# Kernel tuning notes

Hardware: AMD Instinct MI355X
Metric: run time of the kernel (lower is better)

## Reference

```python
import jax, jax.numpy as jnp
import numpy as np

N, E = 20000, 320000
IN, HID, H, C, DFF, L = 256, 64, 4, 64, 128, 4  # per-head dim C = out_channels, concat width = H*C


def _init(k, shape, fan):
    return jax.random.normal(k, shape, jnp.float32) / np.float32(np.sqrt(fan))


def setup_inputs() -> dict:
    key = jax.random.key(0)
    ks = jax.random.split(key, 10)
    x = jax.random.normal(ks[0], (N, IN), jnp.float32)
    edge_index = jax.random.randint(ks[1], (2, E), 0, N)
    We = _init(ks[2], (IN, HID), IN)
    be = jnp.zeros((HID,), jnp.float32)
    Wc = _init(ks[3], (L, HID, H * C), HID)
    att_src = _init(ks[4], (L, H, C), C)
    att_dst = _init(ks[5], (L, H, C), C)
    bc = jnp.zeros((L, H * C), jnp.float32)
    W1 = _init(ks[6], (L, H * C, DFF), H * C)
    b1 = jnp.zeros((L, DFF), jnp.float32)
    W2 = _init(ks[7], (L, DFF, HID), DFF)
    b2 = jnp.zeros((L, HID), jnp.float32)
    ln_g = jnp.ones((L, HID), jnp.float32)
    ln_b = jnp.zeros((L, HID), jnp.float32)
    return dict(x=x, edge_index=edge_index, We=We, be=be, Wc=Wc, att_src=att_src,
                att_dst=att_dst, bc=bc, W1=W1, b1=b1, W2=W2, b2=b2, ln_g=ln_g, ln_b=ln_b)


def _layernorm(x, g, b, eps=1e-5):
    m = x.mean(-1, keepdims=True)
    v = ((x - m) ** 2).mean(-1, keepdims=True)
    return (x - m) / jnp.sqrt(v + eps) * g + b


def reference(x, edge_index, We, be, Wc, att_src, att_dst, bc, W1, b1, W2, b2, ln_g, ln_b):
    # dropout omitted (eval mode)
    n = x.shape[0]
    loops = jnp.arange(n, dtype=edge_index.dtype)
    src = jnp.concatenate([edge_index[0], loops])  # GATConv add_self_loops=True
    dst = jnp.concatenate([edge_index[1], loops])
    h = (x @ We + be) * jnp.sqrt(jnp.float32(HID))  # embed * sqrt(hidden)
    for l in range(L):  # small fixed layer loop
        xh = (h @ Wc[l]).reshape(n, H, C)          # [n,H,C]
        a_s = (xh * att_src[l]).sum(-1)            # [n,H]
        a_d = (xh * att_dst[l]).sum(-1)
        e = a_s[src] + a_d[dst]                    # [E+n,H]
        e = jnp.where(e > 0, e, 0.2 * e)           # leaky_relu(0.2)
        m = jax.ops.segment_max(e, dst, num_segments=n)
        e = jnp.exp(e - m[dst])
        z = jax.ops.segment_sum(e, dst, num_segments=n)
        alpha = e / (z[dst] + 1e-16)               # segment softmax over incoming edges
        msg = xh[src] * alpha[:, :, None]          # [E+n,H,C]
        out = jax.ops.segment_sum(msg, dst, num_segments=n).reshape(n, H * C) + bc[l]
        f = jax.nn.gelu(out @ W1[l] + b1[l], approximate=False) @ W2[l] + b2[l]
        h = h + _layernorm(f, ln_g[l], ln_b[l])    # residual
    return h  # last_hidden_state (head is None)
```

## Files before the change

kernel.cpp:

```cpp
#include <hip/hip_runtime.h>
#include <cmath>

#define NN   20000
#define NE   320000
#define IND  256
#define HIDD 64
#define NH   4
#define CD   64
#define HC   256
#define DFFD 128
#define NL   4


static __device__ __forceinline__ float lrelu(float v) { return v > 0.f ? v : 0.2f * v; }
static __device__ __forceinline__ float wsum(float v) { for (int k = 32; k; k >>= 1) v += __shfl_xor(v, k); return v; }
static __device__ __forceinline__ float wmax(float v) { for (int k = 32; k; k >>= 1) v = fmaxf(v, __shfl_xor(v, k)); return v; }

__global__ void ws_kernel(const float* __restrict__ Wc, const float* __restrict__ att_src,
                          const float* __restrict__ att_dst, float* __restrict__ ws_all) {
    int idx = blockIdx.x * 256 + threadIdx.x;
    int l = idx >> 9, r = (idx >> 6) & 7, k = idx & 63;
    int hh = r & 3;
    const float* att = ((r & 4) ? att_dst : att_src) + (size_t)l * NH * CD + hh * CD;
    const float* wrow = Wc + (size_t)l * HIDD * HC + (size_t)k * HC + hh * CD;
    float s = 0.f;
    for (int c = 0; c < CD; ++c) s += wrow[c] * att[c];
    ws_all[idx] = s;
}

__global__ void w1eff_kernel(const float* __restrict__ Wc, const float* __restrict__ W1,
                             float* __restrict__ W1eff) {
    const int b = blockIdx.x;
    const int l = b >> 8, hk = b & 255, hh = hk >> 6, kl = hk & 63;
    const int f = threadIdx.x;
    const float* wc = Wc + (size_t)l * HIDD * HC + (size_t)kl * HC + hh * 64;
    const float* w1 = W1 + (size_t)l * HC * DFFD + (size_t)(hh * 64) * DFFD + f;
    float s = 0.f;
#pragma unroll 4
    for (int c = 0; c < 64; ++c) s += wc[c] * w1[(size_t)c * DFFD];
    W1eff[(size_t)l * HC * DFFD + (size_t)hk * DFFD + f] = s;
}

__global__ void b1eff_kernel(const float* __restrict__ bc, const float* __restrict__ W1,
                             const float* __restrict__ b1, float* __restrict__ b1eff) {
    const int l = blockIdx.x, f = threadIdx.x;
    const float* w1 = W1 + (size_t)l * HC * DFFD + f;
    const float* bcl = bc + (size_t)l * HC;
    float s = b1[(size_t)l * DFFD + f];
    for (int c = 0; c < HC; ++c) s += bcl[c] * w1[(size_t)c * DFFD];
    b1eff[l * DFFD + f] = s;
}

__global__ __launch_bounds__(256) void embed_kernel(const float* __restrict__ x,
                                                    const float* __restrict__ We,
                                                    const float* __restrict__ be,
                                                    const float* __restrict__ ws_all,
                                                    float* __restrict__ h,
                                                    float* __restrict__ a_s, float* __restrict__ a_d) {
    __shared__ float s_x[16 * IND];
    const int base = blockIdx.x * 16, t = threadIdx.x;
    for (int idx = t; idx < 16 * IND / 4; idx += 256)
        ((float4*)s_x)[idx] = ((const float4*)(x + (size_t)base * IND))[idx];
    __syncthreads();
    const int c = t & 63, g = t >> 6;
    float acc[4] = {0.f, 0.f, 0.f, 0.f};
    const float4* sx4 = (const float4*)s_x;
#pragma unroll 2
    for (int k4 = 0; k4 < IND / 4; ++k4) {
        float w0 = We[(4 * k4 + 0) * HIDD + c];
        float w1 = We[(4 * k4 + 1) * HIDD + c];
        float w2 = We[(4 * k4 + 2) * HIDD + c];
        float w3 = We[(4 * k4 + 3) * HIDD + c];
#pragma unroll
        for (int i = 0; i < 4; ++i) {
            float4 v = sx4[(4 * g + i) * (IND / 4) + k4];
            acc[i] += v.x * w0 + v.y * w1 + v.z * w2 + v.w * w3;
        }
    }
    float bias = be[c];
    float wr[8];
#pragma unroll
    for (int r = 0; r < 8; ++r) wr[r] = ws_all[r * 64 + c];
#pragma unroll
    for (int i = 0; i < 4; ++i) {
        int node = base + 4 * g + i;
        float hv = (acc[i] + bias) * 8.0f;
        h[(size_t)node * HIDD + c] = hv;
        float s0 = wsum(hv * wr[0]), s1 = wsum(hv * wr[1]);
        float s2 = wsum(hv * wr[2]), s3 = wsum(hv * wr[3]);
        float s4 = wsum(hv * wr[4]), s5 = wsum(hv * wr[5]);
        float s6 = wsum(hv * wr[6]), s7 = wsum(hv * wr[7]);
        if (c == 0) {
            ((float4*)a_s)[node] = make_float4(s0, s1, s2, s3);
            ((float4*)a_d)[node] = make_float4(s4, s5, s6, s7);
        }
    }
}

__global__ void init_deg(int* __restrict__ deg, int* __restrict__ cursor) {
    int i = blockIdx.x * blockDim.x + threadIdx.x;
    if (i < NN) { deg[i] = 1; cursor[i] = 0; }
}

__global__ void count_edges(const int* __restrict__ ei, int* __restrict__ deg) {
    int e = blockIdx.x * blockDim.x + threadIdx.x;
    if (e < NE) atomicAdd(&deg[ei[NE + e]], 1);
}

__global__ void scan_kernel(const int* __restrict__ deg, int* __restrict__ rowptr) {
    __shared__ int part[1024];
    const int t = threadIdx.x;
    const int CH = (NN + 1023) / 1024;
    int lo = t * CH, hi = lo + CH; if (hi > NN) hi = NN;
    int s = 0;
    for (int i = lo; i < hi; ++i) s += deg[i];
    part[t] = s;
    __syncthreads();
    for (int off = 1; off < 1024; off <<= 1) {
        int v = 0;
        if (t >= off) v = part[t - off];
        __syncthreads();
        if (t >= off) part[t] += v;
        __syncthreads();
    }
    int base = (t == 0) ? 0 : part[t - 1];
    for (int i = lo; i < hi; ++i) { rowptr[i] = base; base += deg[i]; }
    if (lo <= NN - 1 && NN - 1 < hi) rowptr[NN] = base;
}

__global__ void scatter_edges(const int* __restrict__ ei, const int* __restrict__ rowptr,
                              int* __restrict__ cursor, int* __restrict__ csr_src) {
    int e = blockIdx.x * blockDim.x + threadIdx.x;
    if (e < NE) {
        int s = ei[e], d = ei[NE + e];
        int pos = atomicAdd(&cursor[d], 1);
        csr_src[rowptr[d] + pos] = s;
    } else if (e < NE + NN) {
        int i = e - NE;
        int pos = atomicAdd(&cursor[i], 1);
        csr_src[rowptr[i] + pos] = i;
    }
}

__global__ __launch_bounds__(256) void agg_kernel(
    const float* __restrict__ h, const float* __restrict__ a_s, const float* __restrict__ a_d,
    const int* __restrict__ rowptr, const int* __restrict__ csr_src,
    float* __restrict__ hagg) {
    __shared__ int    s_src[8][64];
    __shared__ float4 s_w[8][64];
    const int t = threadIdx.x, wave = t >> 6, lane = t & 63;
    const float4* as4 = (const float4*)a_s;
#pragma unroll
    for (int nd = 0; nd < 2; ++nd) {
        const int slot = wave * 2 + nd;
        const int i = blockIdx.x * 8 + slot;
        const int lo = rowptr[i], n = rowptr[i + 1] - lo;
        const float4 ad = ((const float4*)a_d)[i];
        float acc0 = 0.f, acc1 = 0.f, acc2 = 0.f, acc3 = 0.f;
        if (n <= 64) {
            float e0 = -1e30f, e1 = -1e30f, e2 = -1e30f, e3 = -1e30f;
            if (lane < n) {
                int s = csr_src[lo + lane];
                s_src[slot][lane] = s;
                float4 a = as4[s];
                e0 = lrelu(a.x + ad.x); e1 = lrelu(a.y + ad.y);
                e2 = lrelu(a.z + ad.z); e3 = lrelu(a.w + ad.w);
            }
            float M0 = wmax(e0), M1 = wmax(e1), M2 = wmax(e2), M3 = wmax(e3);
            float p0 = __expf(e0 - M0), p1 = __expf(e1 - M1);
            float p2 = __expf(e2 - M2), p3 = __expf(e3 - M3);
            float iz0 = 1.f / (wsum(p0) + 1e-16f), iz1 = 1.f / (wsum(p1) + 1e-16f);
            float iz2 = 1.f / (wsum(p2) + 1e-16f), iz3 = 1.f / (wsum(p3) + 1e-16f);
            if (lane < n) s_w[slot][lane] = make_float4(p0 * iz0, p1 * iz1, p2 * iz2, p3 * iz3);
            int j = 0;
            for (; j + 4 <= n; j += 4) {
                int  q0 = s_src[slot][j],     q1 = s_src[slot][j + 1];
                int  q2 = s_src[slot][j + 2], q3 = s_src[slot][j + 3];
                float h0 = h[(size_t)q0 * HIDD + lane], h1 = h[(size_t)q1 * HIDD + lane];
                float h2 = h[(size_t)q2 * HIDD + lane], h3 = h[(size_t)q3 * HIDD + lane];
                float4 w0 = s_w[slot][j],     w1 = s_w[slot][j + 1];
                float4 w2 = s_w[slot][j + 2], w3 = s_w[slot][j + 3];
                acc0 += h0 * w0.x + h1 * w1.x + h2 * w2.x + h3 * w3.x;
                acc1 += h0 * w0.y + h1 * w1.y + h2 * w2.y + h3 * w3.y;
                acc2 += h0 * w0.z + h1 * w1.z + h2 * w2.z + h3 * w3.z;
                acc3 += h0 * w0.w + h1 * w1.w + h2 * w2.w + h3 * w3.w;
            }
            for (; j < n; ++j) {
                float hv = h[(size_t)s_src[slot][j] * HIDD + lane];
                float4 w = s_w[slot][j];
                acc0 += hv * w.x; acc1 += hv * w.y; acc2 += hv * w.z; acc3 += hv * w.w;
            }
        } else {
            float m0 = -1e30f, m1 = -1e30f, m2 = -1e30f, m3 = -1e30f;
            for (int j = lane; j < n; j += 64) {
                int s = csr_src[lo + j];
                float4 a = as4[s];
                m0 = fmaxf(m0, lrelu(a.x + ad.x)); m1 = fmaxf(m1, lrelu(a.y + ad.y));
                m2 = fmaxf(m2, lrelu(a.z + ad.z)); m3 = fmaxf(m3, lrelu(a.w + ad.w));
            }
            m0 = wmax(m0); m1 = wmax(m1); m2 = wmax(m2); m3 = wmax(m3);
            float z0 = 0.f, z1 = 0.f, z2 = 0.f, z3 = 0.f;
            for (int j = lane; j < n; j += 64) {
                int s = csr_src[lo + j];
                float4 a = as4[s];
                z0 += __expf(lrelu(a.x + ad.x) - m0); z1 += __expf(lrelu(a.y + ad.y) - m1);
                z2 += __expf(lrelu(a.z + ad.z) - m2); z3 += __expf(lrelu(a.w + ad.w) - m3);
            }
            float iz0 = 1.f / (wsum(z0) + 1e-16f), iz1 = 1.f / (wsum(z1) + 1e-16f);
            float iz2 = 1.f / (wsum(z2) + 1e-16f), iz3 = 1.f / (wsum(z3) + 1e-16f);
            for (int cb = 0; cb < n; cb += 64) {
                int nn = n - cb; if (nn > 64) nn = 64;
                if (lane < nn) {
                    int s = csr_src[lo + cb + lane];
                    s_src[slot][lane] = s;
                    float4 a = as4[s];
                    s_w[slot][lane] = make_float4(__expf(lrelu(a.x + ad.x) - m0) * iz0,
                                                  __expf(lrelu(a.y + ad.y) - m1) * iz1,
                                                  __expf(lrelu(a.z + ad.z) - m2) * iz2,
                                                  __expf(lrelu(a.w + ad.w) - m3) * iz3);
                }
                int j = 0;
                for (; j + 4 <= nn; j += 4) {
                    int  q0 = s_src[slot][j],     q1 = s_src[slot][j + 1];
                    int  q2 = s_src[slot][j + 2], q3 = s_src[slot][j + 3];
                    float h0 = h[(size_t)q0 * HIDD + lane], h1 = h[(size_t)q1 * HIDD + lane];
                    float h2 = h[(size_t)q2 * HIDD + lane], h3 = h[(size_t)q3 * HIDD + lane];
                    float4 w0 = s_w[slot][j],     w1 = s_w[slot][j + 1];
                    float4 w2 = s_w[slot][j + 2], w3 = s_w[slot][j + 3];
                    acc0 += h0 * w0.x + h1 * w1.x + h2 * w2.x + h3 * w3.x;
                    acc1 += h0 * w0.y + h1 * w1.y + h2 * w2.y + h3 * w3.y;
                    acc2 += h0 * w0.z + h1 * w1.z + h2 * w2.z + h3 * w3.z;
                    acc3 += h0 * w0.w + h1 * w1.w + h2 * w2.w + h3 * w3.w;
                }
                for (; j < nn; ++j) {
                    float hv = h[(size_t)s_src[slot][j] * HIDD + lane];
                    float4 w = s_w[slot][j];
                    acc0 += hv * w.x; acc1 += hv * w.y; acc2 += hv * w.z; acc3 += hv * w.w;
                }
            }
        }
        float* hg = hagg + (size_t)i * HC;
        hg[0 * 64 + lane] = acc0; hg[1 * 64 + lane] = acc1;
        hg[2 * 64 + lane] = acc2; hg[3 * 64 + lane] = acc3;
    }
}

__global__ __launch_bounds__(256, 3) void ffn_kernel(
    const float* __restrict__ hagg, const float* __restrict__ W1eff, const float* __restrict__ b1eff,
    const float* __restrict__ W2, const float* __restrict__ b2,
    const float* __restrict__ ln_g, const float* __restrict__ ln_b,
    const float* __restrict__ ws_next,
    float* __restrict__ h, float* __restrict__ a_s, float* __restrict__ a_d) {
    __shared__ float s_buf[8192];
    __shared__ float s_in[16 * HC];
    const int base = blockIdx.x * 16, t = threadIdx.x;
    for (int idx = t; idx < 16 * HC / 4; idx += 256)
        ((float4*)s_in)[idx] = ((const float4*)(hagg + (size_t)base * HC))[idx];

    const int f = t & 127, g = t >> 7;
    float acc1[8];
#pragma unroll
    for (int i = 0; i < 8; ++i) acc1[i] = 0.f;
    {
        const float4* si4 = (const float4*)s_in;
        for (int kt = 0; kt < 4; ++kt) {
            __syncthreads();
            const float4* gsrc = (const float4*)(W1eff + (size_t)kt * 64 * DFFD);
            for (int idx = t; idx < 2048; idx += 256)
                ((float4*)s_buf)[idx] = gsrc[idx];
            __syncthreads();
#pragma unroll 4
            for (int k4 = 0; k4 < 16; ++k4) {
                float w0 = s_buf[(4 * k4 + 0) * DFFD + f];
                float w1 = s_buf[(4 * k4 + 1) * DFFD + f];
                float w2 = s_buf[(4 * k4 + 2) * DFFD + f];
                float w3 = s_buf[(4 * k4 + 3) * DFFD + f];
#pragma unroll
                for (int i = 0; i < 8; ++i) {
                    float4 v = si4[(8 * g + i) * 64 + kt * 16 + k4];
                    acc1[i] += v.x * w0 + v.y * w1 + v.z * w2 + v.w * w3;
                }
            }
        }
        __syncthreads();
        float bb = b1eff[f];
#pragma unroll
        for (int i = 0; i < 8; ++i) {
            float d = acc1[i] + bb;
            s_buf[(8 * g + i) * DFFD + f] = 0.5f * d * (1.f + erff(d * 0.70710678118654752f));
        }
    }
    __syncthreads();

    {
        const int lane = t & 63, w = t >> 6;
        float acc[4];
#pragma unroll
        for (int i = 0; i < 4; ++i) acc[i] = 0.f;
        const float4* sm4 = (const float4*)s_buf;
#pragma unroll 4
        for (int k4 = 0; k4 < 32; ++k4) {
            float w0 = W2[(4 * k4 + 0) * HIDD + lane];
            float w1 = W2[(4 * k4 + 1) * HIDD + lane];
            float w2 = W2[(4 * k4 + 2) * HIDD + lane];
            float w3 = W2[(4 * k4 + 3) * HIDD + lane];
#pragma unroll
            for (int i = 0; i < 4; ++i) {
                float4 v = sm4[(4 * w + i) * 32 + k4];
                acc[i] += v.x * w0 + v.y * w1 + v.z * w2 + v.w * w3;
            }
        }
        const float b2c = b2[lane], gc = ln_g[lane], bbc = ln_b[lane];
        float wr[8];
#pragma unroll
        for (int r = 0; r < 8; ++r) wr[r] = 0.f;
        if (ws_next) {
#pragma unroll
            for (int r = 0; r < 8; ++r) wr[r] = ws_next[r * 64 + lane];
        }
#pragma unroll
        for (int i = 0; i < 4; ++i) {
            int node = base + 4 * w + i;
            float d = acc[i] + b2c;
            float mean = wsum(d) * (1.0f / 64.0f);
            float dd = d - mean;
            float var = wsum(dd * dd) * (1.0f / 64.0f);
            float hv = h[(size_t)node * HIDD + lane] + dd * rsqrtf(var + 1e-5f) * gc + bbc;
            h[(size_t)node * HIDD + lane] = hv;
            if (ws_next) {
                float s0 = wsum(hv * wr[0]), s1 = wsum(hv * wr[1]);
                float s2 = wsum(hv * wr[2]), s3 = wsum(hv * wr[3]);
                float s4 = wsum(hv * wr[4]), s5 = wsum(hv * wr[5]);
                float s6 = wsum(hv * wr[6]), s7 = wsum(hv * wr[7]);
                if (lane == 0) {
                    ((float4*)a_s)[node] = make_float4(s0, s1, s2, s3);
                    ((float4*)a_d)[node] = make_float4(s4, s5, s6, s7);
                }
            }
        }
    }
}

__global__ void copy_out(const float* __restrict__ h, float* __restrict__ out) {
    int i = blockIdx.x * blockDim.x + threadIdx.x;
    if (i < NN * HIDD / 4) ((float4*)out)[i] = ((const float4*)h)[i];
}

extern "C" void kernel_launch(void* const* d_in, const int* in_sizes, int n_in,
                              void* d_out, int out_size, void* d_ws, size_t ws_size,
                              hipStream_t stream) {
    const float* x       = (const float*)d_in[0];
    const int*   ei      = (const int*)d_in[1];
    const float* We      = (const float*)d_in[2];
    const float* be      = (const float*)d_in[3];
    const float* Wc      = (const float*)d_in[4];
    const float* att_src = (const float*)d_in[5];
    const float* att_dst = (const float*)d_in[6];
    const float* bc      = (const float*)d_in[7];
    const float* W1      = (const float*)d_in[8];
    const float* b1      = (const float*)d_in[9];
    const float* W2      = (const float*)d_in[10];
    const float* b2      = (const float*)d_in[11];
    const float* ln_g    = (const float*)d_in[12];
    const float* ln_b    = (const float*)d_in[13];

    char* ws = (char*)d_ws;
    size_t off = 0;
    auto alloc = [&](size_t bytes) -> void* {
        void* p = ws + off; off += (bytes + 255) & ~(size_t)255; return p;
    };
    float* h       = (float*)alloc((size_t)NN * HIDD * 4);
    float* hagg    = (float*)alloc((size_t)NN * HC * 4);
    float* a_s     = (float*)alloc((size_t)NN * NH * 4);
    float* a_d     = (float*)alloc((size_t)NN * NH * 4);
    float* ws_all  = (float*)alloc((size_t)NL * 8 * 64 * 4);
    float* W1eff   = (float*)alloc((size_t)NL * HC * DFFD * 4);
    float* b1eff   = (float*)alloc((size_t)NL * DFFD * 4);
    int*   deg     = (int*)alloc((size_t)NN * 4);
    int*   rowptr  = (int*)alloc((size_t)(NN + 1) * 4);
    int*   cursor  = (int*)alloc((size_t)NN * 4);
    int*   csr_src = (int*)alloc((size_t)(NE + NN) * 4);
    (void)ws_size; (void)in_sizes; (void)n_in; (void)out_size;

    ws_kernel<<<8, 256, 0, stream>>>(Wc, att_src, att_dst, ws_all);
    w1eff_kernel<<<NL * 256, 128, 0, stream>>>(Wc, W1, W1eff);
    b1eff_kernel<<<NL, 128, 0, stream>>>(bc, W1, b1, b1eff);
    init_deg<<<(NN + 255) / 256, 256, 0, stream>>>(deg, cursor);
    embed_kernel<<<NN / 16, 256, 0, stream>>>(x, We, be, ws_all, h, a_s, a_d);
    count_edges<<<(NE + 255) / 256, 256, 0, stream>>>(ei, deg);
    scan_kernel<<<1, 1024, 0, stream>>>(deg, rowptr);
    scatter_edges<<<(NE + NN + 255) / 256, 256, 0, stream>>>(ei, rowptr, cursor, csr_src);

    for (int l = 0; l < NL; ++l) {
        agg_kernel<<<NN / 8, 256, 0, stream>>>(h, a_s, a_d, rowptr, csr_src, hagg);
        ffn_kernel<<<NN / 16, 256, 0, stream>>>(hagg,
            W1eff + (size_t)l * HC * DFFD, b1eff + (size_t)l * DFFD,
            W2 + (size_t)l * DFFD * HIDD, b2 + (size_t)l * HIDD,
            ln_g + (size_t)l * HIDD, ln_b + (size_t)l * HIDD,
            (l + 1 < NL) ? (ws_all + (size_t)(l + 1) * 8 * 64) : (const float*)nullptr,
            h, a_s, a_d);
    }
    copy_out<<<(NN * HIDD / 4 + 255) / 256, 256, 0, stream>>>(h, (float*)d_out);
}
```

Before: 565.6 us.

## Fuse attention aggregation into FFN layer kernel with ping-pong buffers

Merges the per-layer aggregation and FFN kernels into one kernel that gathers neighbor features into shared memory and then runs the FFN and layernorm on them. This drops the global hagg buffer write and read. Because other blocks still read h, h and the attention scores now ping-pong between two buffers, and the last layer writes straight to the output, which removes the final copy. The W1 inner loop is also re-tiled to float4 weights with 2 rows per thread. Fewer resident waves are available during the irregular gather phase, since the fused kernel uses more shared memory and has a min-blocks launch bound.

```diff
diff --git a/kernel.cpp b/kernel.cpp
--- a/kernel.cpp
+++ b/kernel.cpp
@@ -142,158 +142,161 @@
     }
 }
 
-__global__ __launch_bounds__(256) void agg_kernel(
-    const float* __restrict__ h, const float* __restrict__ a_s, const float* __restrict__ a_d,
+__global__ __launch_bounds__(256, 3) void layer_kernel(
+    const float* __restrict__ h_in, const float* __restrict__ a_s_in, const float* __restrict__ a_d_in,
     const int* __restrict__ rowptr, const int* __restrict__ csr_src,
-    float* __restrict__ hagg) {
-    __shared__ int    s_src[8][64];
-    __shared__ float4 s_w[8][64];
-    const int t = threadIdx.x, wave = t >> 6, lane = t & 63;
-    const float4* as4 = (const float4*)a_s;
-#pragma unroll
-    for (int nd = 0; nd < 2; ++nd) {
-        const int slot = wave * 2 + nd;
-        const int i = blockIdx.x * 8 + slot;
-        const int lo = rowptr[i], n = rowptr[i + 1] - lo;
-        const float4 ad = ((const float4*)a_d)[i];
-        float acc0 = 0.f, acc1 = 0.f, acc2 = 0.f, acc3 = 0.f;
-        if (n <= 64) {
-            float e0 = -1e30f, e1 = -1e30f, e2 = -1e30f, e3 = -1e30f;
-            if (lane < n) {
-                int s = csr_src[lo + lane];
-                s_src[slot][lane] = s;
-                float4 a = as4[s];
-                e0 = lrelu(a.x + ad.x); e1 = lrelu(a.y + ad.y);
-                e2 = lrelu(a.z + ad.z); e3 = lrelu(a.w + ad.w);
-            }
-            float M0 = wmax(e0), M1 = wmax(e1), M2 = wmax(e2), M3 = wmax(e3);
-            float p0 = __expf(e0 - M0), p1 = __expf(e1 - M1);
-            float p2 = __expf(e2 - M2), p3 = __expf(e3 - M3);
-            float iz0 = 1.f / (wsum(p0) + 1e-16f), iz1 = 1.f / (wsum(p1) + 1e-16f);
-            float iz2 = 1.f / (wsum(p2) + 1e-16f), iz3 = 1.f / (wsum(p3) + 1e-16f);
-            if (lane < n) s_w[slot][lane] = make_float4(p0 * iz0, p1 * iz1, p2 * iz2, p3 * iz3);
-            int j = 0;
-            for (; j + 4 <= n; j += 4) {
-                int  q0 = s_src[slot][j],     q1 = s_src[slot][j + 1];
-                int  q2 = s_src[slot][j + 2], q3 = s_src[slot][j + 3];
-                float h0 = h[(size_t)q0 * HIDD + lane], h1 = h[(size_t)q1 * HIDD + lane];
-                float h2 = h[(size_t)q2 * HIDD + lane], h3 = h[(size_t)q3 * HIDD + lane];
-                float4 w0 = s_w[slot][j],     w1 = s_w[slot][j + 1];
-                float4 w2 = s_w[slot][j + 2], w3 = s_w[slot][j + 3];
-                acc0 += h0 * w0.x + h1 * w1.x + h2 * w2.x + h3 * w3.x;
-                acc1 += h0 * w0.y + h1 * w1.y + h2 * w2.y + h3 * w3.y;
-                acc2 += h0 * w0.z + h1 * w1.z + h2 * w2.z + h3 * w3.z;
-                acc3 += h0 * w0.w + h1 * w1.w + h2 * w2.w + h3 * w3.w;
-            }
-            for (; j < n; ++j) {
-                float hv = h[(size_t)s_src[slot][j] * HIDD + lane];
-                float4 w = s_w[slot][j];
-                acc0 += hv * w.x; acc1 += hv * w.y; acc2 += hv * w.z; acc3 += hv * w.w;
-            }
-        } else {
-            float m0 = -1e30f, m1 = -1e30f, m2 = -1e30f, m3 = -1e30f;
-            for (int j = lane; j < n; j += 64) {
-                int s = csr_src[lo + j];
-                float4 a = as4[s];
-                m0 = fmaxf(m0, lrelu(a.x + ad.x)); m1 = fmaxf(m1, lrelu(a.y + ad.y));
-                m2 = fmaxf(m2, lrelu(a.z + ad.z)); m3 = fmaxf(m3, lrelu(a.w + ad.w));
-            }
-            m0 = wmax(m0); m1 = wmax(m1); m2 = wmax(m2); m3 = wmax(m3);
-            float z0 = 0.f, z1 = 0.f, z2 = 0.f, z3 = 0.f;
-            for (int j = lane; j < n; j += 64) {
-                int s = csr_src[lo + j];
-                float4 a = as4[s];
-                z0 += __expf(lrelu(a.x + ad.x) - m0); z1 += __expf(lrelu(a.y + ad.y) - m1);
-                z2 += __expf(lrelu(a.z + ad.z) - m2); z3 += __expf(lrelu(a.w + ad.w) - m3);
-            }
-            float iz0 = 1.f / (wsum(z0) + 1e-16f), iz1 = 1.f / (wsum(z1) + 1e-16f);
-            float iz2 = 1.f / (wsum(z2) + 1e-16f), iz3 = 1.f / (wsum(z3) + 1e-16f);
-            for (int cb = 0; cb < n; cb += 64) {
-                int nn = n - cb; if (nn > 64) nn = 64;
-                if (lane < nn) {
-                    int s = csr_src[lo + cb + lane];
-                    s_src[slot][lane] = s;
-                    float4 a = as4[s];
-                    s_w[slot][lane] = make_float4(__expf(lrelu(a.x + ad.x) - m0) * iz0,
-                                                  __expf(lrelu(a.y + ad.y) - m1) * iz1,
-                                                  __expf(lrelu(a.z + ad.z) - m2) * iz2,
-                                                  __expf(lrelu(a.w + ad.w) - m3) * iz3);
-                }
-                int j = 0;
-                for (; j + 4 <= nn; j += 4) {
-                    int  q0 = s_src[slot][j],     q1 = s_src[slot][j + 1];
-                    int  q2 = s_src[slot][j + 2], q3 = s_src[slot][j + 3];
-                    float h0 = h[(size_t)q0 * HIDD + lane], h1 = h[(size_t)q1 * HIDD + lane];
-                    float h2 = h[(size_t)q2 * HIDD + lane], h3 = h[(size_t)q3 * HIDD + lane];
-                    float4 w0 = s_w[slot][j],     w1 = s_w[slot][j + 1];
-                    float4 w2 = s_w[slot][j + 2], w3 = s_w[slot][j + 3];
-                    acc0 += h0 * w0.x + h1 * w1.x + h2 * w2.x + h3 * w3.x;
-                    acc1 += h0 * w0.y + h1 * w1.y + h2 * w2.y + h3 * w3.y;
-                    acc2 += h0 * w0.z + h1 * w1.z + h2 * w2.z + h3 * w3.z;
-                    acc3 += h0 * w0.w + h1 * w1.w + h2 * w2.w + h3 * w3.w;
-                }
-                for (; j < nn; ++j) {
-                    float hv = h[(size_t)s_src[slot][j] * HIDD + lane];
-                    float4 w = s_w[slot][j];
-                    acc0 += hv * w.x; acc1 += hv * w.y; acc2 += hv * w.z; acc3 += hv * w.w;
-                }
-            }
-        }
-        float* hg = hagg + (size_t)i * HC;
-        hg[0 * 64 + lane] = acc0; hg[1 * 64 + lane] = acc1;
-        hg[2 * 64 + lane] = acc2; hg[3 * 64 + lane] = acc3;
-    }
-}
-
-__global__ __launch_bounds__(256, 3) void ffn_kernel(
-    const float* __restrict__ hagg, const float* __restrict__ W1eff, const float* __restrict__ b1eff,
+    const float* __restrict__ W1eff, const float* __restrict__ b1eff,
     const float* __restrict__ W2, const float* __restrict__ b2,
     const float* __restrict__ ln_g, const float* __restrict__ ln_b,
     const float* __restrict__ ws_next,
-    float* __restrict__ h, float* __restrict__ a_s, float* __restrict__ a_d) {
+    float* __restrict__ h_out, float* __restrict__ a_s_out, float* __restrict__ a_d_out) {
+    __shared__ float s_in[16 * HC];
     __shared__ float s_buf[8192];
-    __shared__ float s_in[16 * HC];
-    const int base = blockIdx.x * 16, t = threadIdx.x;
-    for (int idx = t; idx < 16 * HC / 4; idx += 256)
-        ((float4*)s_in)[idx] = ((const float4*)(hagg + (size_t)base * HC))[idx];
-
-    const int f = t & 127, g = t >> 7;
-    float acc1[8];
-#pragma unroll
-    for (int i = 0; i < 8; ++i) acc1[i] = 0.f;
+    const int base = blockIdx.x * 16, t = threadIdx.x, wave = t >> 6, lane = t & 63;
+
+    {
+        int*    s_src = (int*)s_buf + wave * 64;
+        float4* s_w   = (float4*)(s_buf + 256) + wave * 64;
+        const float4* as4 = (const float4*)a_s_in;
+        for (int nd = 0; nd < 4; ++nd) {
+            const int node = base + wave * 4 + nd;
+            const int lo = rowptr[node], n = rowptr[node + 1] - lo;
+            const float4 ad = ((const float4*)a_d_in)[node];
+            float g0 = 0.f, g1 = 0.f, g2 = 0.f, g3 = 0.f;
+            if (n <= 64) {
+                float e0 = -1e30f, e1 = -1e30f, e2 = -1e30f, e3 = -1e30f;
+                if (lane < n) {
+                    int s = csr_src[lo + lane];
+                    s_src[lane] = s;
+                    float4 a = as4[s];
+                    e0 = lrelu(a.x + ad.x); e1 = lrelu(a.y + ad.y);
+                    e2 = lrelu(a.z + ad.z); e3 = lrelu(a.w + ad.w);
+                }
+                float M0 = wmax(e0), M1 = wmax(e1), M2 = wmax(e2), M3 = wmax(e3);
+                float p0 = __expf(e0 - M0), p1 = __expf(e1 - M1);
+                float p2 = __expf(e2 - M2), p3 = __expf(e3 - M3);
+                float iz0 = 1.f / (wsum(p0) + 1e-16f), iz1 = 1.f / (wsum(p1) + 1e-16f);
+                float iz2 = 1.f / (wsum(p2) + 1e-16f), iz3 = 1.f / (wsum(p3) + 1e-16f);
+                if (lane < n) s_w[lane] = make_float4(p0 * iz0, p1 * iz1, p2 * iz2, p3 * iz3);
+                int j = 0;
+                for (; j + 4 <= n; j += 4) {
+                    int  q0 = s_src[j], q1 = s_src[j + 1], q2 = s_src[j + 2], q3 = s_src[j + 3];
+                    float h0 = h_in[(size_t)q0 * HIDD + lane], h1 = h_in[(size_t)q1 * HIDD + lane];
+                    float h2 = h_in[(size_t)q2 * HIDD + lane], h3 = h_in[(size_t)q3 * HIDD + lane];
+                    float4 w0 = s_w[j], w1 = s_w[j + 1], w2 = s_w[j + 2], w3 = s_w[j + 3];
+                    g0 += h0 * w0.x + h1 * w1.x + h2 * w2.x + h3 * w3.x;
+                    g1 += h0 * w0.y + h1 * w1.y + h2 * w2.y + h3 * w3.y;
+                    g2 += h0 * w0.z + h1 * w1.z + h2 * w2.z + h3 * w3.z;
+                    g3 += h0 * w0.w + h1 * w1.w + h2 * w2.w + h3 * w3.w;
+                }
+                for (; j < n; ++j) {
+                    float hv = h_in[(size_t)s_src[j] * HIDD + lane];
+                    float4 w = s_w[j];
+                    g0 += hv * w.x; g1 += hv * w.y; g2 += hv * w.z; g3 += hv * w.w;
+                }
+            } else {
+                float m0 = -1e30f, m1 = -1e30f, m2 = -1e30f, m3 = -1e30f;
+                for (int j = lane; j < n; j += 64) {
+                    int s = csr_src[lo + j];
+                    float4 a = as4[s];
+                    m0 = fmaxf(m0, lrelu(a.x + ad.x)); m1 = fmaxf(m1, lrelu(a.y + ad.y));
+                    m2 = fmaxf(m2, lrelu(a.z + ad.z)); m3 = fmaxf(m3, lrelu(a.w + ad.w));
+                }
+                m0 = wmax(m0); m1 = wmax(m1); m2 = wmax(m2); m3 = wmax(m3);
+                float z0 = 0.f, z1 = 0.f, z2 = 0.f, z3 = 0.f;
+                for (int j = lane; j < n; j += 64) {
+                    int s = csr_src[lo + j];
+                    float4 a = as4[s];
+                    z0 += __expf(lrelu(a.x + ad.x) - m0); z1 += __expf(lrelu(a.y + ad.y) - m1);
+                    z2 += __expf(lrelu(a.z + ad.z) - m2); z3 += __expf(lrelu(a.w + ad.w) - m3);
+                }
+                float iz0 = 1.f / (wsum(z0) + 1e-16f), iz1 = 1.f / (wsum(z1) + 1e-16f);
+                float iz2 = 1.f / (wsum(z2) + 1e-16f), iz3 = 1.f / (wsum(z3) + 1e-16f);
+                for (int cb = 0; cb < n; cb += 64) {
+                    int nn = n - cb; if (nn > 64) nn = 64;
+                    if (lane < nn) {
+                        int s = csr_src[lo + cb + lane];
+                        s_src[lane] = s;
+                        float4 a = as4[s];
+                        s_w[lane] = make_float4(__expf(lrelu(a.x + ad.x) - m0) * iz0,
+                                                __expf(lrelu(a.y + ad.y) - m1) * iz1,
+                                                __expf(lrelu(a.z + ad.z) - m2) * iz2,
+                                                __expf(lrelu(a.w + ad.w) - m3) * iz3);
+                    }
+                    int j = 0;
+                    for (; j + 4 <= nn; j += 4) {
+                        int  q0 = s_src[j], q1 = s_src[j + 1], q2 = s_src[j + 2], q3 = s_src[j + 3];
+                        float h0 = h_in[(size_t)q0 * HIDD + lane], h1 = h_in[(size_t)q1 * HIDD + lane];
+                        float h2 = h_in[(size_t)q2 * HIDD + lane], h3 = h_in[(size_t)q3 * HIDD + lane];
+                        float4 w0 = s_w[j], w1 = s_w[j + 1], w2 = s_w[j + 2], w3 = s_w[j + 3];
+                        g0 += h0 * w0.x + h1 * w1.x + h2 * w2.x + h3 * w3.x;
+                        g1 += h0 * w0.y + h1 * w1.y + h2 * w2.y + h3 * w3.y;
+                        g2 += h0 * w0.z + h1 * w1.z + h2 * w2.z + h3 * w3.z;
+                        g3 += h0 * w0.w + h1 * w1.w + h2 * w2.w + h3 * w3.w;
+                    }
+                    for (; j < nn; ++j) {
+                        float hv = h_in[(size_t)s_src[j] * HIDD + lane];
+                        float4 w = s_w[j];
+                        g0 += hv * w.x; g1 += hv * w.y; g2 += hv * w.z; g3 += hv * w.w;
+                    }
+                }
+            }
+            const int r = wave * 4 + nd;
+            s_in[r * HC + 0 * 64 + lane] = g0;
+            s_in[r * HC + 1 * 64 + lane] = g1;
+            s_in[r * HC + 2 * 64 + lane] = g2;
+            s_in[r * HC + 3 * 64 + lane] = g3;
+        }
+    }
+    __syncthreads();
+
+    const int fg = t & 31, ng2 = t >> 5;
+    float4 acc1[2];
+    acc1[0] = make_float4(0.f, 0.f, 0.f, 0.f);
+    acc1[1] = make_float4(0.f, 0.f, 0.f, 0.f);
     {
         const float4* si4 = (const float4*)s_in;
+        float4* sB4 = (float4*)s_buf;
         for (int kt = 0; kt < 4; ++kt) {
             __syncthreads();
             const float4* gsrc = (const float4*)(W1eff + (size_t)kt * 64 * DFFD);
-            for (int idx = t; idx < 2048; idx += 256)
-                ((float4*)s_buf)[idx] = gsrc[idx];
+            for (int idx = t; idx < 2048; idx += 256) sB4[idx] = gsrc[idx];
             __syncthreads();
 #pragma unroll 4
             for (int k4 = 0; k4 < 16; ++k4) {
-                float w0 = s_buf[(4 * k4 + 0) * DFFD + f];
-                float w1 = s_buf[(4 * k4 + 1) * DFFD + f];
-                float w2 = s_buf[(4 * k4 + 2) * DFFD + f];
-                float w3 = s_buf[(4 * k4 + 3) * DFFD + f];
-#pragma unroll
-                for (int i = 0; i < 8; ++i) {
-                    float4 v = si4[(8 * g + i) * 64 + kt * 16 + k4];
-                    acc1[i] += v.x * w0 + v.y * w1 + v.z * w2 + v.w * w3;
+                float4 w0 = sB4[(4 * k4 + 0) * 32 + fg];
+                float4 w1 = sB4[(4 * k4 + 1) * 32 + fg];
+                float4 w2 = sB4[(4 * k4 + 2) * 32 + fg];
+                float4 w3 = sB4[(4 * k4 + 3) * 32 + fg];
+#pragma unroll
+                for (int i = 0; i < 2; ++i) {
+                    float4 v = si4[(2 * ng2 + i) * 64 + kt * 16 + k4];
+                    acc1[i].x += v.x * w0.x + v.y * w1.x + v.z * w2.x + v.w * w3.x;
+                    acc1[i].y += v.x * w0.y + v.y * w1.y + v.z * w2.y + v.w * w3.y;
+                    acc1[i].z += v.x * w0.z + v.y * w1.z + v.z * w2.z + v.w * w3.z;
+                    acc1[i].w += v.x * w0.w + v.y * w1.w + v.z * w2.w + v.w * w3.w;
                 }
             }
         }
-        __syncthreads();
-        float bb = b1eff[f];
-#pragma unroll
-        for (int i = 0; i < 8; ++i) {
-            float d = acc1[i] + bb;
-            s_buf[(8 * g + i) * DFFD + f] = 0.5f * d * (1.f + erff(d * 0.70710678118654752f));
-        }
     }
     __syncthreads();
-
     {
-        const int lane = t & 63, w = t >> 6;
+        float4 bb = *(const float4*)(b1eff + 4 * fg);
+#pragma unroll
+        for (int i = 0; i < 2; ++i) {
+            float dx = acc1[i].x + bb.x, dy = acc1[i].y + bb.y;
+            float dz = acc1[i].z + bb.z, dw = acc1[i].w + bb.w;
+            ((float4*)s_buf)[(2 * ng2 + i) * 32 + fg] = make_float4(
+                0.5f * dx * (1.f + erff(dx * 0.70710678118654752f)),
+                0.5f * dy * (1.f + erff(dy * 0.70710678118654752f)),
+                0.5f * dz * (1.f + erff(dz * 0.70710678118654752f)),
+                0.5f * dw * (1.f + erff(dw * 0.70710678118654752f)));
+        }
+    }
+    __syncthreads();
+
+    {
+        const int w = t >> 6;
         float acc[4];
 #pragma unroll
         for (int i = 0; i < 4; ++i) acc[i] = 0.f;
@@ -325,25 +328,20 @@
             float mean = wsum(d) * (1.0f / 64.0f);
             float dd = d - mean;
             float var = wsum(dd * dd) * (1.0f / 64.0f);
-            float hv = h[(size_t)node * HIDD + lane] + dd * rsqrtf(var + 1e-5f) * gc + bbc;
-            h[(size_t)node * HIDD + lane] = hv;
+            float hv = h_in[(size_t)node * HIDD + lane] + dd * rsqrtf(var + 1e-5f) * gc + bbc;
+            h_out[(size_t)node * HIDD + lane] = hv;
             if (ws_next) {
                 float s0 = wsum(hv * wr[0]), s1 = wsum(hv * wr[1]);
                 float s2 = wsum(hv * wr[2]), s3 = wsum(hv * wr[3]);
                 float s4 = wsum(hv * wr[4]), s5 = wsum(hv * wr[5]);
                 float s6 = wsum(hv * wr[6]), s7 = wsum(hv * wr[7]);
                 if (lane == 0) {
-                    ((float4*)a_s)[node] = make_float4(s0, s1, s2, s3);
-                    ((float4*)a_d)[node] = make_float4(s4, s5, s6, s7);
+                    ((float4*)a_s_out)[node] = make_float4(s0, s1, s2, s3);
+                    ((float4*)a_d_out)[node] = make_float4(s4, s5, s6, s7);
                 }
             }
         }
     }
-}
-
-__global__ void copy_out(const float* __restrict__ h, float* __restrict__ out) {
-    int i = blockIdx.x * blockDim.x + threadIdx.x;
-    if (i < NN * HIDD / 4) ((float4*)out)[i] = ((const float4*)h)[i];
 }
 
 extern "C" void kernel_launch(void* const* d_in, const int* in_sizes, int n_in,
@@ -369,10 +367,12 @@
     auto alloc = [&](size_t bytes) -> void* {
         void* p = ws + off; off += (bytes + 255) & ~(size_t)255; return p;
     };
-    float* h       = (float*)alloc((size_t)NN * HIDD * 4);
-    float* hagg    = (float*)alloc((size_t)NN * HC * 4);
-    float* a_s     = (float*)alloc((size_t)NN * NH * 4);
-    float* a_d     = (float*)alloc((size_t)NN * NH * 4);
+    float* h0      = (float*)alloc((size_t)NN * HIDD * 4);
+    float* h1      = (float*)alloc((size_t)NN * HIDD * 4);
+    float* as0     = (float*)alloc((size_t)NN * NH * 4);
+    float* ad0     = (float*)alloc((size_t)NN * NH * 4);
+    float* as1     = (float*)alloc((size_t)NN * NH * 4);
+    float* ad1     = (float*)alloc((size_t)NN * NH * 4);
     float* ws_all  = (float*)alloc((size_t)NL * 8 * 64 * 4);
     float* W1eff   = (float*)alloc((size_t)NL * HC * DFFD * 4);
     float* b1eff   = (float*)alloc((size_t)NL * DFFD * 4);
@@ -386,19 +386,23 @@
     w1eff_kernel<<<NL * 256, 128, 0, stream>>>(Wc, W1, W1eff);
     b1eff_kernel<<<NL, 128, 0, stream>>>(bc, W1, b1, b1eff);
     init_deg<<<(NN + 255) / 256, 256, 0, stream>>>(deg, cursor);
-    embed_kernel<<<NN / 16, 256, 0, stream>>>(x, We, be, ws_all, h, a_s, a_d);
+    embed_kernel<<<NN / 16, 256, 0, stream>>>(x, We, be, ws_all, h0, as0, ad0);
     count_edges<<<(NE + 255) / 256, 256, 0, stream>>>(ei, deg);
     scan_kernel<<<1, 1024, 0, stream>>>(deg, rowptr);
     scatter_edges<<<(NE + NN + 255) / 256, 256, 0, stream>>>(ei, rowptr, cursor, csr_src);
 
     for (int l = 0; l < NL; ++l) {
-        agg_kernel<<<NN / 8, 256, 0, stream>>>(h, a_s, a_d, rowptr, csr_src, hagg);
-        ffn_kernel<<<NN / 16, 256, 0, stream>>>(hagg,
+        const float* hi  = (l & 1) ? h1  : h0;
+        const float* asi = (l & 1) ? as1 : as0;
+        const float* adi = (l & 1) ? ad1 : ad0;
+        float* ho  = (l == NL - 1) ? (float*)d_out : ((l & 1) ? h0 : h1);
+        float* aso = (l & 1) ? as0 : as1;
+        float* ado = (l & 1) ? ad0 : ad1;
+        layer_kernel<<<NN / 16, 256, 0, stream>>>(hi, asi, adi, rowptr, csr_src,
             W1eff + (size_t)l * HC * DFFD, b1eff + (size_t)l * DFFD,
             W2 + (size_t)l * DFFD * HIDD, b2 + (size_t)l * HIDD,
             ln_g + (size_t)l * HIDD, ln_b + (size_t)l * HIDD,
             (l + 1 < NL) ? (ws_all + (size_t)(l + 1) * 8 * 64) : (const float*)nullptr,
-            h, a_s, a_d);
-    }
-    copy_out<<<(NN * HIDD / 4 + 255) / 256, 256, 0, stream>>>(h, (float*)d_out);
-}
+            ho, aso, ado);
+    }
+}
```

After: 509.2 us. -10.0%, faster.
